# Performance work log

Hardware: AMD Instinct MI355X
Metric: run time of the kernel (lower is better)

The kernel has to match this reference:

```python
import jax, jax.numpy as jnp
import numpy as np

T, N, H, W = 1, 2048, 512, 512
CHUNK = 128  # gaussians per scan step; intermediate alpha is (CHUNK,H,W) ~ 128MB fp32


def setup_inputs() -> dict:
    key = jax.random.key(0)
    k1, k2, k3, k4 = jax.random.split(key, 4)
    # matches torch init: atanh(2*(rand-0.5)) so tanh(xyz) is uniform in (-1,1)
    u = jax.random.uniform(k1, (T, N, 2), dtype=jnp.float32, minval=1e-4, maxval=1.0 - 1e-4)
    xyz = jnp.arctanh(2.0 * (u - 0.5))
    # cholesky params near identity: [1,0,1] + 0.01*randn
    cholesky = jnp.array([1.0, 0.0, 1.0], jnp.float32).reshape(1, 1, 3) \
        + 0.01 * jax.random.normal(k2, (T, N, 3), dtype=jnp.float32)
    opacity = jnp.ones((N, 1), jnp.float32)
    features_dc = jax.random.normal(k4, (N, 3), dtype=jnp.float32)
    return {"xyz": xyz, "cholesky": cholesky, "opacity": opacity,
            "features_dc": features_dc, "frame_index": 0}


def _render_frame(means, chol, colors, opac):
    """Accumulated-summation 2D Gaussian splat (GaussianImage rasterize_gaussians_sum).

    means: (N,2) in (-1,1); chol: (N,3) Cholesky elems (l11,l21,l22);
    colors: (N,3) in (0,1); opac: (N,) in (0,1). Returns (3,H,W).
    """
    l1, l2, l3 = chol[:, 0], chol[:, 1], chol[:, 2]
    # Sigma = L L^T with L = [[l1,0],[l2,l3]]
    s11 = l1 * l1
    s12 = l1 * l2
    s22 = l2 * l2 + l3 * l3
    det = s11 * s22 - s12 * s12
    conic = jnp.stack([s22 / det, -s12 / det, s11 / det], axis=-1)  # (N,3) inverse cov
    # project to pixel coords
    xys = 0.5 * (means + 1.0) * jnp.array([W, H], means.dtype)  # (N,2)

    px = jnp.arange(W, dtype=means.dtype) + 0.5  # pixel centers
    py = jnp.arange(H, dtype=means.dtype) + 0.5

    steps = N // CHUNK
    xs = (xys.reshape(steps, CHUNK, 2), conic.reshape(steps, CHUNK, 3),
          colors.reshape(steps, CHUNK, 3), opac.reshape(steps, CHUNK))

    def body(img, args):
        xy, cc, col, op = args
        dx = xy[:, 0, None] - px[None, :]          # (C,W)
        dy = xy[:, 1, None] - py[None, :]          # (C,H)
        sigma = (0.5 * cc[:, 0, None, None] * (dx[:, None, :] ** 2)
                 + 0.5 * cc[:, 2, None, None] * (dy[:, :, None] ** 2)
                 + cc[:, 1, None, None] * dy[:, :, None] * dx[:, None, :])  # (C,H,W)
        alpha = op[:, None, None] * jnp.exp(-sigma)
        alpha = jnp.where(sigma < 0.0, 0.0, jnp.minimum(alpha, 0.999))
        alpha = jnp.where(alpha < 1.0 / 255.0, 0.0, alpha)  # kernel skip threshold
        img = img + jnp.einsum('chw,ck->khw', alpha, col)
        return img, None

    img0 = jnp.zeros((3, H, W), means.dtype)
    img, _ = jax.lax.scan(body, img0, xs)
    return img


def reference(xyz, cholesky, opacity, features_dc, frame_index):
    cholesky_bound = jnp.array([0.5, 0.0, 0.5], xyz.dtype)
    means_t = jnp.tanh(xyz[frame_index])                       # (N,2)
    chol_t = cholesky[frame_index] + cholesky_bound            # (N,3)
    colors = jax.nn.sigmoid(features_dc)                       # (N,3)
    opac = jax.nn.sigmoid(opacity[:, 0])                       # (N,)
    img = _render_frame(means_t, chol_t, colors, opac)
    img = jnp.clip(img, 0.0, 1.0)
    return img[None]  # (1,3,H,W)
```

## Files before the change

### kernel.cpp

```cpp
#include <hip/hip_runtime.h>
#include <math.h>

#define N_GAUSS 2048
#define IMG_H 512
#define IMG_W 512

__global__ void zero_kernel(float4* __restrict__ out, int n4) {
    int i = blockIdx.x * blockDim.x + threadIdx.x;
    if (i < n4) out[i] = make_float4(0.f, 0.f, 0.f, 0.f);
}

__global__ __launch_bounds__(64) void splat_kernel(
    const float* __restrict__ xyz,
    const float* __restrict__ chol,
    const float* __restrict__ opacity,
    const float* __restrict__ fdc,
    float* __restrict__ out)
{
    const int g = blockIdx.x;
    const int lane = threadIdx.x;

    float mx = tanhf(xyz[2 * g]);
    float my = tanhf(xyz[2 * g + 1]);
    float l1 = chol[3 * g]     + 0.5f;
    float l2 = chol[3 * g + 1];
    float l3 = chol[3 * g + 2] + 0.5f;

    float s11 = l1 * l1;
    float s12 = l1 * l2;
    float s22 = l2 * l2 + l3 * l3;
    float det = s11 * s22 - s12 * s12;
    float inv = 1.0f / det;
    float c0 =  s22 * inv;
    float c1 = -s12 * inv;
    float c2 =  s11 * inv;

    float cx = 0.5f * (mx + 1.0f) * (float)IMG_W;
    float cy = 0.5f * (my + 1.0f) * (float)IMG_H;

    float op = 1.0f / (1.0f + expf(-opacity[g]));
    float cr = 1.0f / (1.0f + expf(-fdc[3 * g]));
    float cg = 1.0f / (1.0f + expf(-fdc[3 * g + 1]));
    float cb = 1.0f / (1.0f + expf(-fdc[3 * g + 2]));

    float s_max = logf(255.0f * op);
    if (s_max < 0.0f) return;

    float rx = sqrtf(2.0f * s_max * s11) + 1.0f;
    float ry = sqrtf(2.0f * s_max * s22) + 1.0f;

    int w0 = max(0,         (int)floorf(cx - rx - 0.5f));
    int w1 = min(IMG_W - 1, (int)ceilf (cx + rx - 0.5f));
    int h0 = max(0,         (int)floorf(cy - ry - 0.5f));
    int h1 = min(IMG_H - 1, (int)ceilf (cy + ry - 0.5f));
    if (w1 < w0 || h1 < h0) return;

    int bw  = w1 - w0 + 1;
    int bh  = h1 - h0 + 1;
    int tot = bw * bh;

    for (int idx = lane; idx < tot; idx += 64) {
        int h = h0 + idx / bw;
        int w = w0 + idx % bw;
        float dx = cx - ((float)w + 0.5f);
        float dy = cy - ((float)h + 0.5f);
        float sigma = 0.5f * c0 * dx * dx + 0.5f * c2 * dy * dy + c1 * dy * dx;
        if (sigma < 0.0f) continue;
        float alpha = fminf(op * expf(-sigma), 0.999f);
        if (alpha < (1.0f / 255.0f)) continue;
        int p = h * IMG_W + w;
        atomicAdd(&out[0 * IMG_H * IMG_W + p], alpha * cr);
        atomicAdd(&out[1 * IMG_H * IMG_W + p], alpha * cg);
        atomicAdd(&out[2 * IMG_H * IMG_W + p], alpha * cb);
    }
}

__global__ void clip_kernel(float4* __restrict__ out, int n4) {
    int i = blockIdx.x * blockDim.x + threadIdx.x;
    if (i < n4) {
        float4 v = out[i];
        v.x = fminf(fmaxf(v.x, 0.0f), 1.0f);
        v.y = fminf(fmaxf(v.y, 0.0f), 1.0f);
        v.z = fminf(fmaxf(v.z, 0.0f), 1.0f);
        v.w = fminf(fmaxf(v.w, 0.0f), 1.0f);
        out[i] = v;
    }
}

extern "C" void kernel_launch(void* const* d_in, const int* in_sizes, int n_in,
                              void* d_out, int out_size, void* d_ws, size_t ws_size,
                              hipStream_t stream) {
    const float* xyz     = (const float*)d_in[0];
    const float* chol    = (const float*)d_in[1];
    const float* opacity = (const float*)d_in[2];
    const float* fdc     = (const float*)d_in[3];

    float* out = (float*)d_out;
    int n4 = out_size / 4;

    zero_kernel<<<(n4 + 255) / 256, 256, 0, stream>>>((float4*)out, n4);
    splat_kernel<<<N_GAUSS, 64, 0, stream>>>(xyz, chol, opacity, fdc, out);
    clip_kernel<<<(n4 + 255) / 256, 256, 0, stream>>>((float4*)out, n4);
}
```

Baseline: 70.96 us.

## Replace gaussian-parallel atomic splat with tile-parallel gather rasterizer

Switches from one block per gaussian doing global atomicAdds to one block per 64x8 pixel tile. Each tile culls gaussians chunk by chunk into shared memory by bounding-box overlap, then every pixel accumulates colour in registers. The zero and clip kernels are folded in, leaving a single launch. Every tile recomputes the per-gaussian preprocessing (tanh, sigmoid, log), and the order of float summation changes.

```diff
diff --git a/kernel.cpp b/kernel.cpp
--- a/kernel.cpp
+++ b/kernel.cpp
@@ -5,86 +5,107 @@
 #define IMG_H 512
 #define IMG_W 512
 
-__global__ void zero_kernel(float4* __restrict__ out, int n4) {
-    int i = blockIdx.x * blockDim.x + threadIdx.x;
-    if (i < n4) out[i] = make_float4(0.f, 0.f, 0.f, 0.f);
-}
+#define TILE_W 64
+#define TILE_H 8
+#define NTHREADS (TILE_W * TILE_H)
+#define CHUNK_G 512
+#define N_CHUNKS (N_GAUSS / CHUNK_G)
 
-__global__ __launch_bounds__(64) void splat_kernel(
+__global__ __launch_bounds__(NTHREADS) void fused_splat_kernel(
     const float* __restrict__ xyz,
     const float* __restrict__ chol,
     const float* __restrict__ opacity,
     const float* __restrict__ fdc,
     float* __restrict__ out)
 {
-    const int g = blockIdx.x;
-    const int lane = threadIdx.x;
+    __shared__ float s_cx[CHUNK_G], s_cy[CHUNK_G];
+    __shared__ float s_h0[CHUNK_G], s_c1[CHUNK_G], s_h2[CHUNK_G];
+    __shared__ float s_op[CHUNK_G];
+    __shared__ float s_cr[CHUNK_G], s_cg[CHUNK_G], s_cb[CHUNK_G];
+    __shared__ int   s_cnt;
 
-    float mx = tanhf(xyz[2 * g]);
-    float my = tanhf(xyz[2 * g + 1]);
-    float l1 = chol[3 * g]     + 0.5f;
-    float l2 = chol[3 * g + 1];
-    float l3 = chol[3 * g + 2] + 0.5f;
+    const int tid = threadIdx.x;
+    const int x = blockIdx.x * TILE_W + (tid & (TILE_W - 1));
+    const int y = blockIdx.y * TILE_H + (tid >> 6);
+    const float wf = (float)x + 0.5f;
+    const float hf = (float)y + 0.5f;
 
-    float s11 = l1 * l1;
-    float s12 = l1 * l2;
-    float s22 = l2 * l2 + l3 * l3;
-    float det = s11 * s22 - s12 * s12;
-    float inv = 1.0f / det;
-    float c0 =  s22 * inv;
-    float c1 = -s12 * inv;
-    float c2 =  s11 * inv;
+    const int tx0 = blockIdx.x * TILE_W;
+    const int tx1 = tx0 + TILE_W - 1;
+    const int ty0 = blockIdx.y * TILE_H;
+    const int ty1 = ty0 + TILE_H - 1;
 
-    float cx = 0.5f * (mx + 1.0f) * (float)IMG_W;
-    float cy = 0.5f * (my + 1.0f) * (float)IMG_H;
+    float accr = 0.f, accg = 0.f, accb = 0.f;
 
-    float op = 1.0f / (1.0f + expf(-opacity[g]));
-    float cr = 1.0f / (1.0f + expf(-fdc[3 * g]));
-    float cg = 1.0f / (1.0f + expf(-fdc[3 * g + 1]));
-    float cb = 1.0f / (1.0f + expf(-fdc[3 * g + 2]));
+    for (int c = 0; c < N_CHUNKS; ++c) {
+        __syncthreads();
+        if (tid == 0) s_cnt = 0;
+        __syncthreads();
 
-    float s_max = logf(255.0f * op);
-    if (s_max < 0.0f) return;
+        const int g = c * CHUNK_G + tid;
+        float mx = tanhf(xyz[2 * g]);
+        float my = tanhf(xyz[2 * g + 1]);
+        float l1 = chol[3 * g]     + 0.5f;
+        float l2 = chol[3 * g + 1];
+        float l3 = chol[3 * g + 2] + 0.5f;
 
-    float rx = sqrtf(2.0f * s_max * s11) + 1.0f;
-    float ry = sqrtf(2.0f * s_max * s22) + 1.0f;
+        float s11 = l1 * l1;
+        float s12 = l1 * l2;
+        float s22 = l2 * l2 + l3 * l3;
+        float det = s11 * s22 - s12 * s12;
+        float inv = 1.0f / det;
+        float c0 =  s22 * inv;
+        float c1 = -s12 * inv;
+        float c2 =  s11 * inv;
 
-    int w0 = max(0,         (int)floorf(cx - rx - 0.5f));
-    int w1 = min(IMG_W - 1, (int)ceilf (cx + rx - 0.5f));
-    int h0 = max(0,         (int)floorf(cy - ry - 0.5f));
-    int h1 = min(IMG_H - 1, (int)ceilf (cy + ry - 0.5f));
-    if (w1 < w0 || h1 < h0) return;
+        float cx = 0.5f * (mx + 1.0f) * (float)IMG_W;
+        float cy = 0.5f * (my + 1.0f) * (float)IMG_H;
 
-    int bw  = w1 - w0 + 1;
-    int bh  = h1 - h0 + 1;
-    int tot = bw * bh;
+        float op = 1.0f / (1.0f + expf(-opacity[g]));
+        float s_max = logf(255.0f * op);
 
-    for (int idx = lane; idx < tot; idx += 64) {
-        int h = h0 + idx / bw;
-        int w = w0 + idx % bw;
-        float dx = cx - ((float)w + 0.5f);
-        float dy = cy - ((float)h + 0.5f);
-        float sigma = 0.5f * c0 * dx * dx + 0.5f * c2 * dy * dy + c1 * dy * dx;
-        if (sigma < 0.0f) continue;
-        float alpha = fminf(op * expf(-sigma), 0.999f);
-        if (alpha < (1.0f / 255.0f)) continue;
-        int p = h * IMG_W + w;
-        atomicAdd(&out[0 * IMG_H * IMG_W + p], alpha * cr);
-        atomicAdd(&out[1 * IMG_H * IMG_W + p], alpha * cg);
-        atomicAdd(&out[2 * IMG_H * IMG_W + p], alpha * cb);
+        bool take = (s_max >= 0.0f);
+        if (take) {
+            float rx = sqrtf(2.0f * s_max * s11) + 1.0f;
+            float ry = sqrtf(2.0f * s_max * s22) + 1.0f;
+            int w0 = (int)floorf(cx - rx - 0.5f);
+            int w1 = (int)ceilf (cx + rx - 0.5f);
+            int h0 = (int)floorf(cy - ry - 0.5f);
+            int h1 = (int)ceilf (cy + ry - 0.5f);
+            take = (w1 >= tx0) && (w0 <= tx1) && (h1 >= ty0) && (h0 <= ty1);
+        }
+        if (take) {
+            int k = atomicAdd(&s_cnt, 1);
+            s_cx[k] = cx;
+            s_cy[k] = cy;
+            s_h0[k] = 0.5f * c0;
+            s_c1[k] = c1;
+            s_h2[k] = 0.5f * c2;
+            s_op[k] = op;
+            s_cr[k] = 1.0f / (1.0f + expf(-fdc[3 * g]));
+            s_cg[k] = 1.0f / (1.0f + expf(-fdc[3 * g + 1]));
+            s_cb[k] = 1.0f / (1.0f + expf(-fdc[3 * g + 2]));
+        }
+        __syncthreads();
+
+        const int n = s_cnt;
+        for (int j = 0; j < n; ++j) {
+            float dx = s_cx[j] - wf;
+            float dy = s_cy[j] - hf;
+            float sigma = s_h0[j] * dx * dx + s_h2[j] * dy * dy + s_c1[j] * dy * dx;
+            if (sigma < 0.0f) continue;
+            float alpha = fminf(s_op[j] * expf(-sigma), 0.999f);
+            if (alpha < (1.0f / 255.0f)) continue;
+            accr += alpha * s_cr[j];
+            accg += alpha * s_cg[j];
+            accb += alpha * s_cb[j];
+        }
     }
-}
 
-__global__ void clip_kernel(float4* __restrict__ out, int n4) {
-    int i = blockIdx.x * blockDim.x + threadIdx.x;
-    if (i < n4) {
-        float4 v = out[i];
-        v.x = fminf(fmaxf(v.x, 0.0f), 1.0f);
-        v.y = fminf(fmaxf(v.y, 0.0f), 1.0f);
-        v.z = fminf(fmaxf(v.z, 0.0f), 1.0f);
-        v.w = fminf(fmaxf(v.w, 0.0f), 1.0f);
-        out[i] = v;
-    }
+    const int p = y * IMG_W + x;
+    out[0 * IMG_H * IMG_W + p] = fminf(fmaxf(accr, 0.0f), 1.0f);
+    out[1 * IMG_H * IMG_W + p] = fminf(fmaxf(accg, 0.0f), 1.0f);
+    out[2 * IMG_H * IMG_W + p] = fminf(fmaxf(accb, 0.0f), 1.0f);
 }
 
 extern "C" void kernel_launch(void* const* d_in, const int* in_sizes, int n_in,
@@ -96,9 +117,7 @@
     const float* fdc     = (const float*)d_in[3];
 
     float* out = (float*)d_out;
-    int n4 = out_size / 4;
 
-    zero_kernel<<<(n4 + 255) / 256, 256, 0, stream>>>((float4*)out, n4);
-    splat_kernel<<<N_GAUSS, 64, 0, stream>>>(xyz, chol, opacity, fdc, out);
-    clip_kernel<<<(n4 + 255) / 256, 256, 0, stream>>>((float4*)out, n4);
+    dim3 grid(IMG_W / TILE_W, IMG_H / TILE_H);
+    fused_splat_kernel<<<grid, NTHREADS, 0, stream>>>(xyz, chol, opacity, fdc, out);
 }
```

New measurement: 73.52 us. 1.04x slower.
